# Optimization experiments

Hardware: AMD Instinct MI355X
Metric: run time of the kernel (lower is better)

## Reference

```python
import jax, jax.numpy as jnp
import numpy as np

N = 100000      # nodes
E = 1600000     # edges
IN_C = 128
HID = 64
OUT_C = 40
LAYERS = 8
ALPHA = 0.1
THETA = 0.5
BN_EPS = 1e-5


def setup_inputs() -> dict:
    key = jax.random.key(0)
    ks = jax.random.split(key, 8)
    x = jax.random.normal(ks[0], (N, IN_C), jnp.float32)
    edge_index = jax.random.randint(ks[1], (2, E), 0, N, dtype=jnp.int64)
    W0 = jax.random.normal(ks[2], (IN_C, HID), jnp.float32) / np.sqrt(IN_C).astype(np.float32)
    b0 = jnp.zeros((HID,), jnp.float32)
    convW = jax.random.normal(ks[3], (LAYERS, HID, HID), jnp.float32) / np.sqrt(HID).astype(np.float32)
    bn_gamma = jnp.ones((LAYERS, HID), jnp.float32)
    bn_beta = jnp.zeros((LAYERS, HID), jnp.float32)
    W_out = jax.random.normal(ks[4], (HID, OUT_C), jnp.float32) / np.sqrt(HID).astype(np.float32)
    b_out = jnp.zeros((OUT_C,), jnp.float32)
    return dict(x=x, edge_index=edge_index, W0=W0, b0=b0, convW=convW,
                bn_gamma=bn_gamma, bn_beta=bn_beta, W_out=W_out, b_out=b_out)


def _gcn_norm(edge_index, n):
    # gcn_norm with improved=False, add_self_loops=True (pyg default)
    loop = jnp.arange(n, dtype=edge_index.dtype)
    row = jnp.concatenate([edge_index[0], loop])
    col = jnp.concatenate([edge_index[1], loop])
    deg = jnp.zeros((n,), jnp.float32).at[col].add(1.0)  # deg >= 1 (self loops)
    dinv = jax.lax.rsqrt(deg)
    w = dinv[row] * dinv[col]
    return row, col, w


def reference(x, edge_index, W0, b0, convW, bn_gamma, bn_beta, W_out, b_out):
    n = x.shape[0]
    row, col, w = _gcn_norm(edge_index, n)
    # dropout in eval mode -> identity
    h = jax.nn.relu(x @ W0 + b0)
    h0 = h
    for i in range(LAYERS):
        beta = float(np.log(THETA / (i + 1) + 1.0))  # GCN2Conv beta for layer i+1
        # adj_t @ h: adj_t = transpose of normalized adjacency -> out[col] += w * h[row]
        agg = jnp.zeros_like(h).at[col].add(w[:, None] * h[row])
        s = (1.0 - ALPHA) * agg + ALPHA * h0              # initial residual
        s = (1.0 - beta) * s + beta * (s @ convW[i])      # identity mapping (shared_weights)
        mu = s.mean(axis=0)
        var = s.var(axis=0)                               # batchnorm (batch stats, biased var)
        s = (s - mu) * jax.lax.rsqrt(var + BN_EPS) * bn_gamma[i] + bn_beta[i]
        h = jax.nn.relu(s)
    return h @ W_out + b_out
```

## Files before the change

kernel.cpp:

```cpp
#include <hip/hip_runtime.h>
#include <math.h>

#define NTHREADS 256
#define IN_C 128
#define HID 64
#define OUT_C 40
#define N_LAYERS 8
#define ALPHA 0.1f
#define BN_EPS 1e-5f
#define BKT_SHIFT 9

typedef float f32x4 __attribute__((ext_vector_type(4)));
typedef _Float16 f16;
typedef _Float16 f16x4 __attribute__((ext_vector_type(4)));
typedef _Float16 f16x8 __attribute__((ext_vector_type(8)));

__device__ __forceinline__ f32x4 ld4(const float* p) { return *(const f32x4*)p; }

__device__ __forceinline__ f32x4 ldh4(const f16* p) {
  f16x4 v = *(const f16x4*)p;
  return __builtin_convertvector(v, f32x4);
}

__device__ __forceinline__ f32x4 bnrelu(f32x4 v, f32x4 k1, f32x4 k2) {
  f32x4 r = v * k1 + k2;
  r.x = fmaxf(r.x, 0.f); r.y = fmaxf(r.y, 0.f);
  r.z = fmaxf(r.z, 0.f); r.w = fmaxf(r.w, 0.f);
  return r;
}

__device__ __forceinline__ f32x4 xreduce(f32x4 v) {
  v.x += __shfl_xor(v.x, 16); v.y += __shfl_xor(v.y, 16);
  v.z += __shfl_xor(v.z, 16); v.w += __shfl_xor(v.w, 16);
  v.x += __shfl_xor(v.x, 32); v.y += __shfl_xor(v.y, 32);
  v.z += __shfl_xor(v.z, 32); v.w += __shfl_xor(v.w, 32);
  return v;
}


__global__ void k_zero(float* __restrict__ sumP, float* __restrict__ sumsqP,
                       f16* __restrict__ svpad, int* __restrict__ bcnt) {
  int i = blockIdx.x * NTHREADS + threadIdx.x;
  if (i < N_LAYERS * 1024) { sumP[i] = 0.f; sumsqP[i] = 0.f; }
  if (i < 256) {
    f16x4 z = {(f16)0.f, (f16)0.f, (f16)0.f, (f16)0.f};
    ((f16x4*)svpad)[i] = z;
  }
  if (blockIdx.x == 0 && threadIdx.x < 256) bcnt[threadIdx.x] = 0;
}

__global__ __launch_bounds__(NTHREADS) void k_bhist(
    const int* __restrict__ col, int* __restrict__ bcnt, int E, int nb) {
  __shared__ int lhist[512];
  int t = threadIdx.x;
  for (int i = t; i < nb; i += NTHREADS) lhist[i] = 0;
  __syncthreads();
  int start = blockIdx.x * 4096;
  int end = min(E, start + 4096);
  for (int e = start + t; e < end; e += NTHREADS)
    atomicAdd(&lhist[col[e] >> BKT_SHIFT], 1);
  __syncthreads();
  for (int i = t; i < nb; i += NTHREADS) {
    int c = lhist[i];
    if (c) atomicAdd(&bcnt[i], c);
  }
}

__global__ void k_bscan(const int* __restrict__ bcnt, int* __restrict__ bbase,
                        int* __restrict__ bcur, int* __restrict__ offs,
                        int nb, int n, int E) {
  __shared__ int sh[256];
  int t = threadIdx.x;
  int v = (t < nb) ? bcnt[t] : 0;
  sh[t] = v;
  __syncthreads();
  int run = v;
  for (int d = 1; d < 256; d <<= 1) {
    int add = (t >= d) ? sh[t - d] : 0;
    __syncthreads();
    run += add;
    sh[t] = run;
    __syncthreads();
  }
  if (t < nb) {
    bbase[t] = run - v;
    bcur[t] = run - v;
  }
  if (t == 0) {
    bbase[nb] = E;
    offs[n] = E;
  }
}

__global__ __launch_bounds__(NTHREADS) void k_bucketA(
    const int* __restrict__ row, const int* __restrict__ col,
    int* __restrict__ bcur, long long* __restrict__ tmp, int E, int nb) {
  __shared__ int lhist[512];
  __shared__ int lbase[512];
  int t = threadIdx.x;
  for (int i = t; i < nb; i += NTHREADS) lhist[i] = 0;
  __syncthreads();
  int start = blockIdx.x * 4096;
  int end = min(E, start + 4096);
  for (int e = start + t; e < end; e += NTHREADS)
    atomicAdd(&lhist[col[e] >> BKT_SHIFT], 1);
  __syncthreads();
  for (int i = t; i < nb; i += NTHREADS) {
    int c = lhist[i];
    lbase[i] = c ? atomicAdd(&bcur[i], c) : 0;
    lhist[i] = 0;
  }
  __syncthreads();
  for (int e = start + t; e < end; e += NTHREADS) {
    int cl = col[e];
    int b = cl >> BKT_SHIFT;
    int slot = atomicAdd(&lhist[b], 1);
    tmp[lbase[b] + slot] = ((long long)cl << 32) | (unsigned int)row[e];
  }
}

__global__ __launch_bounds__(512) void k_bucketB(
    const long long* __restrict__ tmp, const int* __restrict__ bbase,
    int* __restrict__ offs, float* __restrict__ dinv,
    int* __restrict__ ew, int n) {
  __shared__ int lcnt[512];
  __shared__ int lcur[512];
  int b = blockIdx.x;
  int t = threadIdx.x;
  int lo = b << BKT_SHIFT;
  int s = bbase[b], e2 = bbase[b + 1];
  lcnt[t] = 0;
  __syncthreads();
  for (int j = s + t; j < e2; j += 512)
    atomicAdd(&lcnt[(int)(tmp[j] >> 32) - lo], 1);
  __syncthreads();
  int v = lcnt[t];
  int run = v;
  for (int d = 1; d < 512; d <<= 1) {
    int add = (t >= d) ? lcnt[t - d] : 0;
    __syncthreads();
    run += add;
    lcnt[t] = run;
    __syncthreads();
  }
  int node = lo + t;
  int myoff = s + run - v;
  if (node < n) {
    offs[node] = myoff;
    dinv[node] = rsqrtf((float)v + 1.0f);
  }
  lcur[t] = myoff;
  __syncthreads();
  for (int j = s + t; j < e2; j += 512) {
    long long r = tmp[j];
    int cl = (int)(r >> 32);
    int pos = atomicAdd(&lcur[cl - lo], 1);
    ew[pos] = (int)(r & 0xffffffffLL);
  }
}

__global__ void k_gemm0(
    const float* __restrict__ x, const float* __restrict__ W0,
    const float* __restrict__ b0, const float* __restrict__ dinv,
    f16* __restrict__ h016, f16* __restrict__ hp, int n) {
  int t = threadIdx.x;
  int lane = t & 63, wid = t >> 6;
  int lm = lane & 15, lk = lane >> 4;
  f16x8 bf[4][4];
  float bv[4];
#pragma unroll
  for (int nt = 0; nt < 4; nt++) {
    int c = nt * 16 + lm;
    bv[nt] = b0[c];
#pragma unroll
    for (int ks = 0; ks < 4; ks++) {
#pragma unroll
      for (int i = 0; i < 8; i++) {
        bf[nt][ks][i] = (f16)W0[(ks * 32 + lk * 8 + i) * HID + c];
      }
    }
  }
  int nblk = (n + 15) >> 4;
  for (int blk = blockIdx.x * 4 + wid; blk < nblk; blk += gridDim.x * 4) {
    int r0 = blk * 16;
    int rA = min(r0 + lm, n - 1);
    const float* xr = x + (size_t)rA * IN_C + lk * 8;
    f16x8 af[4];
#pragma unroll
    for (int ks = 0; ks < 4; ks++) {
      f32x4 lo = ld4(xr + ks * 32);
      f32x4 hi = ld4(xr + ks * 32 + 4);
      f16x4 l16 = __builtin_convertvector(lo, f16x4);
      f16x4 h16 = __builtin_convertvector(hi, f16x4);
#pragma unroll
      for (int i = 0; i < 4; i++) { af[ks][i] = l16[i]; af[ks][4 + i] = h16[i]; }
    }
    float dv[4];
#pragma unroll
    for (int reg = 0; reg < 4; reg++)
      dv[reg] = dinv[min(r0 + lk * 4 + reg, n - 1)];
#pragma unroll
    for (int nt = 0; nt < 4; nt++) {
      f32x4 z = {0.f, 0.f, 0.f, 0.f};
      z = __builtin_amdgcn_mfma_f32_16x16x32_f16(af[0], bf[nt][0], z, 0, 0, 0);
      z = __builtin_amdgcn_mfma_f32_16x16x32_f16(af[1], bf[nt][1], z, 0, 0, 0);
      z = __builtin_amdgcn_mfma_f32_16x16x32_f16(af[2], bf[nt][2], z, 0, 0, 0);
      z = __builtin_amdgcn_mfma_f32_16x16x32_f16(af[3], bf[nt][3], z, 0, 0, 0);
#pragma unroll
      for (int reg = 0; reg < 4; reg++) {
        int r = r0 + lk * 4 + reg;
        if (r < n) {
          float v = fmaxf(z[reg] + bv[nt], 0.f);
          h016[(size_t)r * HID + nt * 16 + lm] = (f16)v;
          hp[(size_t)r * HID + nt * 16 + lm] = (f16)(dv[reg] * v);
        }
      }
    }
  }
}

__global__ void k_gather(
    const f16* __restrict__ hp, const f16* __restrict__ h0,
    const float* __restrict__ dinv, const int* __restrict__ offs,
    const int* __restrict__ ew, f16* __restrict__ sv, int n) {
  int t = threadIdx.x;
  int lane = t & 63;
  int eg = lane >> 4, li = lane & 15, c4 = li << 2;
  int i = blockIdx.x * 16 + (t >> 6) * 4 + eg;
  if (i >= n) return;
  int jb = offs[i], je = offs[i + 1];
  float di = dinv[i];
  f16x4 hs16 = *(const f16x4*)(hp + (size_t)i * HID + c4);
  f16x4 h016v = *(const f16x4*)(h0 + (size_t)i * HID + c4);
  f32x4 acc = {0.f, 0.f, 0.f, 0.f};
  int j = jb;
  for (; j + 8 <= je; j += 8) {
    int q0 = ew[j + 0];
    int q1 = ew[j + 1];
    int q2 = ew[j + 2];
    int q3 = ew[j + 3];
    int q4 = ew[j + 4];
    int q5 = ew[j + 5];
    int q6 = ew[j + 6];
    int q7 = ew[j + 7];
    f16x4 u0 = *(const f16x4*)(hp + (size_t)q0 * HID + c4);
    f16x4 u1 = *(const f16x4*)(hp + (size_t)q1 * HID + c4);
    f16x4 u2 = *(const f16x4*)(hp + (size_t)q2 * HID + c4);
    f16x4 u3 = *(const f16x4*)(hp + (size_t)q3 * HID + c4);
    f16x4 u4 = *(const f16x4*)(hp + (size_t)q4 * HID + c4);
    f16x4 u5 = *(const f16x4*)(hp + (size_t)q5 * HID + c4);
    f16x4 u6 = *(const f16x4*)(hp + (size_t)q6 * HID + c4);
    f16x4 u7 = *(const f16x4*)(hp + (size_t)q7 * HID + c4);
    acc += __builtin_convertvector(u0, f32x4);
    acc += __builtin_convertvector(u1, f32x4);
    acc += __builtin_convertvector(u2, f32x4);
    acc += __builtin_convertvector(u3, f32x4);
    acc += __builtin_convertvector(u4, f32x4);
    acc += __builtin_convertvector(u5, f32x4);
    acc += __builtin_convertvector(u6, f32x4);
    acc += __builtin_convertvector(u7, f32x4);
  }
  for (; j < je; j++) {
    acc += ldh4(hp + (size_t)ew[j] * HID + c4);
  }
  f32x4 hs = __builtin_convertvector(hs16, f32x4);
  f32x4 h0v = __builtin_convertvector(h016v, f32x4);
  f32x4 sval = (1.f - ALPHA) * (di * (acc + hs)) + ALPHA * h0v;
  *(f16x4*)(sv + (size_t)i * HID + c4) = __builtin_convertvector(sval, f16x4);
}

__global__ __launch_bounds__(NTHREADS) void k_conv(
    const f16* __restrict__ sv, const float* __restrict__ Wl,
    f16* __restrict__ sout, float* __restrict__ sumL,
    float* __restrict__ sumsqL, float beta, int n) {
  __shared__ __align__(16) float Wsh[HID * HID];
  __shared__ f32x4 red4[2][4][16];
  int t = threadIdx.x;
  for (int m = t; m < HID * HID / 4; m += NTHREADS) {
    f32x4 wv = ((const f32x4*)Wl)[m];
    wv *= beta;
    int base = m * 4;
    int k = base >> 6, c0 = base & 63;
    if (k >= c0 && k < c0 + 4) wv[k - c0] += (1.f - beta);
    ((f32x4*)Wsh)[m] = wv;
  }
  __syncthreads();
  int lane = t & 63, wid = t >> 6;
  int lm = lane & 15, lk = lane >> 4;
  f16x8 bf[4][2];
#pragma unroll
  for (int nt = 0; nt < 4; nt++) {
#pragma unroll
    for (int ks = 0; ks < 2; ks++) {
      int c = nt * 16 + lm;
#pragma unroll
      for (int i = 0; i < 8; i++) {
        int k = ks * 32 + lk * 8 + i;
        bf[nt][ks][i] = (f16)Wsh[k * HID + c];
      }
    }
  }
  float ssum[4] = {0.f, 0.f, 0.f, 0.f}, ssq[4] = {0.f, 0.f, 0.f, 0.f};
  int nblk = (n + 15) >> 4;
  for (int blk = blockIdx.x * 4 + wid; blk < nblk; blk += gridDim.x * 4) {
    int r0 = blk * 16;
    const f16* ap = sv + (size_t)(r0 + lm) * HID + lk * 8;
    f16x8 a0 = *(const f16x8*)(ap);
    f16x8 a1 = *(const f16x8*)(ap + 32);
#pragma unroll
    for (int nt = 0; nt < 4; nt++) {
      f32x4 z = {0.f, 0.f, 0.f, 0.f};
      z = __builtin_amdgcn_mfma_f32_16x16x32_f16(a0, bf[nt][0], z, 0, 0, 0);
      z = __builtin_amdgcn_mfma_f32_16x16x32_f16(a1, bf[nt][1], z, 0, 0, 0);
#pragma unroll
      for (int reg = 0; reg < 4; reg++) {
        int r = r0 + lk * 4 + reg;
        if (r < n) {
          float v = z[reg];
          sout[(size_t)r * HID + nt * 16 + lm] = (f16)v;
          ssum[nt] += v;
          ssq[nt] += v * v;
        }
      }
    }
  }
  f32x4 sumv = {ssum[0], ssum[1], ssum[2], ssum[3]};
  f32x4 sqv = {ssq[0], ssq[1], ssq[2], ssq[3]};
  sumv = xreduce(sumv);
  sqv = xreduce(sqv);
  if (lk == 0) { red4[0][wid][lm] = sumv; red4[1][wid][lm] = sqv; }
  __syncthreads();
  if (t < 16) {
    f32x4 a = red4[0][0][t] + red4[0][1][t] + red4[0][2][t] + red4[0][3][t];
    f32x4 b = red4[1][0][t] + red4[1][1][t] + red4[1][2][t] + red4[1][3][t];
    int js = (blockIdx.x & 15) * 64;
    atomicAdd(&sumL[js + 0 * 16 + t], a.x);
    atomicAdd(&sumL[js + 1 * 16 + t], a.y);
    atomicAdd(&sumL[js + 2 * 16 + t], a.z);
    atomicAdd(&sumL[js + 3 * 16 + t], a.w);
    atomicAdd(&sumsqL[js + 0 * 16 + t], b.x);
    atomicAdd(&sumsqL[js + 1 * 16 + t], b.y);
    atomicAdd(&sumsqL[js + 2 * 16 + t], b.z);
    atomicAdd(&sumsqL[js + 3 * 16 + t], b.w);
  }
}

__device__ __forceinline__ void stats_to_lds(
    const float* __restrict__ sumL, const float* __restrict__ sumsqL,
    const float* __restrict__ gamma_l, const float* __restrict__ beta_l,
    float* ms, int t, int n) {
  if (t < 64) {
    float s = 0.f, sq = 0.f;
#pragma unroll
    for (int j = 0; j < 16; j++) {
      s += sumL[j * 64 + t];
      sq += sumsqL[j * 64 + t];
    }
    float mu = s / (float)n;
    float var = sq / (float)n - mu * mu;
    float iv = rsqrtf(var + BN_EPS);
    float k1 = iv * gamma_l[t];
    ms[t] = k1;
    ms[64 + t] = beta_l[t] - mu * k1;
  }
  __syncthreads();
}

__global__ __launch_bounds__(NTHREADS) void k_bnrelu(
    const f16* __restrict__ s, const float* __restrict__ sumL,
    const float* __restrict__ sumsqL, const float* __restrict__ gamma_l,
    const float* __restrict__ beta_l, const float* __restrict__ dinv,
    f16* __restrict__ hp, int n) {
  __shared__ __align__(16) float ms[128];
  int t = threadIdx.x;
  stats_to_lds(sumL, sumsqL, gamma_l, beta_l, ms, t, n);
  int idx = blockIdx.x * NTHREADS + t;
  if (idx < n * (HID / 4)) {
    int c4 = idx & 15;
    int row = idx >> 4;
    f32x4 v = ldh4(s + (size_t)idx * 4);
    f32x4 k1 = *(const f32x4*)(ms + c4 * 4);
    f32x4 k2 = *(const f32x4*)(ms + 64 + c4 * 4);
    v = bnrelu(v, k1, k2);
    float di = dinv[row];
    v = di * v;
    ((f16x4*)hp)[idx] = __builtin_convertvector(v, f16x4);
  }
}

__global__ __launch_bounds__(NTHREADS) void k_out(
    const f16* __restrict__ s, const float* __restrict__ sumL,
    const float* __restrict__ sumsqL, const float* __restrict__ gamma_l,
    const float* __restrict__ beta_l, const float* __restrict__ Wout,
    const float* __restrict__ bout, float* __restrict__ out, int n) {
  __shared__ float Ws[HID * OUT_C];
  __shared__ float bs[OUT_C];
  __shared__ __align__(16) float ms[128];
  int t = threadIdx.x;
  for (int m = t; m < HID * OUT_C; m += NTHREADS) Ws[m] = Wout[m];
  if (t < OUT_C) bs[t] = bout[t];
  stats_to_lds(sumL, sumsqL, gamma_l, beta_l, ms, t, n);
  int idx = blockIdx.x * NTHREADS + t;
  if (idx < n * OUT_C) {
    int row = idx / OUT_C;
    int c = idx - row * OUT_C;
    float acc = bs[c];
    const f16* sr = s + (size_t)row * HID;
    for (int kk = 0; kk < HID / 4; kk++) {
      f32x4 a = ldh4(sr + kk * 4);
      f32x4 k1 = *(const f32x4*)(ms + kk * 4);
      f32x4 k2 = *(const f32x4*)(ms + 64 + kk * 4);
      a = bnrelu(a, k1, k2);
      int k = kk * 4;
      acc += a.x * Ws[(k + 0) * OUT_C + c] + a.y * Ws[(k + 1) * OUT_C + c] +
             a.z * Ws[(k + 2) * OUT_C + c] + a.w * Ws[(k + 3) * OUT_C + c];
    }
    out[idx] = acc;
  }
}


extern "C" void kernel_launch(void* const* d_in, const int* in_sizes, int n_in,
                              void* d_out, int out_size, void* d_ws, size_t ws_size,
                              hipStream_t stream) {
  const float* x = (const float*)d_in[0];
  const int* ei = (const int*)d_in[1];
  const float* W0 = (const float*)d_in[2];
  const float* b0 = (const float*)d_in[3];
  const float* convW = (const float*)d_in[4];
  const float* bn_gamma = (const float*)d_in[5];
  const float* bn_beta = (const float*)d_in[6];
  const float* W_out = (const float*)d_in[7];
  const float* b_out = (const float*)d_in[8];
  float* out = (float*)d_out;

  int n = in_sizes[0] / IN_C;
  int E = in_sizes[1] / 2;
  const int* row = ei;
  const int* col = ei + E;
  int NB = (n + (1 << BKT_SHIFT) - 1) >> BKT_SHIFT;

  char* w = (char*)d_ws;
  auto alloc = [&](size_t bytes) {
    char* p = w;
    w += (bytes + 255) & ~(size_t)255;
    return p;
  };
  float* dinv    = (float*)alloc((size_t)n * 4);
  int*   offs    = (int*)alloc((size_t)(n + 1) * 4);
  int*   bcnt    = (int*)alloc(512 * 4);
  int*   bbase   = (int*)alloc(512 * 4);
  int*   bcur    = (int*)alloc(512 * 4);
  int*   ew      = (int*)alloc((size_t)E * 4);
  long long* tmp = (long long*)alloc((size_t)E * 8);
  f16*   h016    = (f16*)alloc((size_t)n * HID * 2);
  f16*   hp      = (f16*)alloc((size_t)n * HID * 2);
  f16*   sv      = (f16*)alloc((size_t)(n + 16) * HID * 2);
  f16*   sb      = (f16*)alloc((size_t)n * HID * 2);
  float* sumP    = (float*)alloc((size_t)N_LAYERS * 1024 * 4);
  float* sumsqP  = (float*)alloc((size_t)N_LAYERS * 1024 * 4);

  int gE4 = (E + 4095) / 4096;
  int gRow = (n + 15) / 16;
  int gConv = (gRow + 3) / 4;
  int gV = (n * (HID / 4) + NTHREADS - 1) / NTHREADS;

  k_zero<<<33, NTHREADS, 0, stream>>>(sumP, sumsqP, sv + (size_t)n * HID, bcnt);
  k_bhist<<<gE4, NTHREADS, 0, stream>>>(col, bcnt, E, NB);
  k_bscan<<<1, 256, 0, stream>>>(bcnt, bbase, bcur, offs, NB, n, E);
  k_bucketA<<<gE4, NTHREADS, 0, stream>>>(row, col, bcur, tmp, E, NB);
  k_bucketB<<<NB, 512, 0, stream>>>(tmp, bbase, offs, dinv, ew, n);

  k_gemm0<<<512, NTHREADS, 0, stream>>>(x, W0, b0, dinv, h016, hp, n);

  for (int l = 0; l < N_LAYERS; l++) {
    float beta = logf(0.5f / (float)(l + 1) + 1.0f);
    if (l > 0) {
      k_bnrelu<<<gV, NTHREADS, 0, stream>>>(
          sb, sumP + (size_t)(l - 1) * 1024, sumsqP + (size_t)(l - 1) * 1024,
          bn_gamma + (l - 1) * HID, bn_beta + (l - 1) * HID, dinv, hp, n);
    }
    k_gather<<<gRow, NTHREADS, 0, stream>>>(hp, h016, dinv, offs, ew, sv, n);
    k_conv<<<gConv, NTHREADS, 0, stream>>>(sv, convW + (size_t)l * HID * HID,
                                           sb, sumP + (size_t)l * 1024,
                                           sumsqP + (size_t)l * 1024, beta, n);
  }

  k_out<<<((size_t)n * OUT_C + NTHREADS - 1) / NTHREADS, NTHREADS, 0, stream>>>(
      sb, sumP + (size_t)7 * 1024, sumsqP + (size_t)7 * 1024,
      bn_gamma + 7 * HID, bn_beta + 7 * HID, W_out, b_out, out, n);
}
```

Baseline: 693.1 us.

## Compute output projection with MFMA f16 instead of scalar per-element loop

Rewrites the final output kernel so each wavefront handles 16-row blocks and computes the 64x40 projection with mfma_f32_16x16x32_f16, keeping W_out fragments in registers. The old version used one thread per output element, re-reading the row of s and W_out from LDS 64 times per output. The new version also launches a grid-stride kernel with the conv grid size. In exchange, W_out and the post-BN activations are rounded to f16 before the multiply, which costs some precision, and it pads 40 columns up to 48.

```diff
diff --git a/kernel.cpp b/kernel.cpp
--- a/kernel.cpp
+++ b/kernel.cpp
@@ -393,29 +393,61 @@
     const float* __restrict__ sumsqL, const float* __restrict__ gamma_l,
     const float* __restrict__ beta_l, const float* __restrict__ Wout,
     const float* __restrict__ bout, float* __restrict__ out, int n) {
-  __shared__ float Ws[HID * OUT_C];
-  __shared__ float bs[OUT_C];
   __shared__ __align__(16) float ms[128];
   int t = threadIdx.x;
-  for (int m = t; m < HID * OUT_C; m += NTHREADS) Ws[m] = Wout[m];
-  if (t < OUT_C) bs[t] = bout[t];
   stats_to_lds(sumL, sumsqL, gamma_l, beta_l, ms, t, n);
-  int idx = blockIdx.x * NTHREADS + t;
-  if (idx < n * OUT_C) {
-    int row = idx / OUT_C;
-    int c = idx - row * OUT_C;
-    float acc = bs[c];
-    const f16* sr = s + (size_t)row * HID;
-    for (int kk = 0; kk < HID / 4; kk++) {
-      f32x4 a = ldh4(sr + kk * 4);
-      f32x4 k1 = *(const f32x4*)(ms + kk * 4);
-      f32x4 k2 = *(const f32x4*)(ms + 64 + kk * 4);
-      a = bnrelu(a, k1, k2);
-      int k = kk * 4;
-      acc += a.x * Ws[(k + 0) * OUT_C + c] + a.y * Ws[(k + 1) * OUT_C + c] +
-             a.z * Ws[(k + 2) * OUT_C + c] + a.w * Ws[(k + 3) * OUT_C + c];
-    }
-    out[idx] = acc;
+  int lane = t & 63, wid = t >> 6;
+  int lm = lane & 15, lk = lane >> 4;
+  f16x8 bf[3][2];
+  float bv[3];
+#pragma unroll
+  for (int nt = 0; nt < 3; nt++) {
+    int c = nt * 16 + lm;
+    bv[nt] = (c < OUT_C) ? bout[c] : 0.f;
+#pragma unroll
+    for (int ks = 0; ks < 2; ks++) {
+#pragma unroll
+      for (int i = 0; i < 8; i++) {
+        int k = ks * 32 + lk * 8 + i;
+        bf[nt][ks][i] = (c < OUT_C) ? (f16)Wout[k * OUT_C + c] : (f16)0.f;
+      }
+    }
+  }
+  float k1a[8], k2a[8], k1b[8], k2b[8];
+#pragma unroll
+  for (int i = 0; i < 8; i++) {
+    k1a[i] = ms[lk * 8 + i];
+    k2a[i] = ms[64 + lk * 8 + i];
+    k1b[i] = ms[32 + lk * 8 + i];
+    k2b[i] = ms[64 + 32 + lk * 8 + i];
+  }
+  int nblk = (n + 15) >> 4;
+  for (int blk = blockIdx.x * 4 + wid; blk < nblk; blk += gridDim.x * 4) {
+    int r0 = blk * 16;
+    int rA = min(r0 + lm, n - 1);
+    const f16* sr = s + (size_t)rA * HID + lk * 8;
+    f16x8 s0 = *(const f16x8*)(sr);
+    f16x8 s1 = *(const f16x8*)(sr + 32);
+    f16x8 a0, a1;
+#pragma unroll
+    for (int i = 0; i < 8; i++) {
+      a0[i] = (f16)fmaxf((float)s0[i] * k1a[i] + k2a[i], 0.f);
+      a1[i] = (f16)fmaxf((float)s1[i] * k1b[i] + k2b[i], 0.f);
+    }
+#pragma unroll
+    for (int nt = 0; nt < 3; nt++) {
+      int c = nt * 16 + lm;
+      f32x4 z = {0.f, 0.f, 0.f, 0.f};
+      z = __builtin_amdgcn_mfma_f32_16x16x32_f16(a0, bf[nt][0], z, 0, 0, 0);
+      z = __builtin_amdgcn_mfma_f32_16x16x32_f16(a1, bf[nt][1], z, 0, 0, 0);
+#pragma unroll
+      for (int reg = 0; reg < 4; reg++) {
+        int r = r0 + lk * 4 + reg;
+        if (r < n && c < OUT_C) {
+          out[(size_t)r * OUT_C + c] = z[reg] + bv[nt];
+        }
+      }
+    }
   }
 }
 
@@ -486,7 +518,7 @@
                                            sumsqP + (size_t)l * 1024, beta, n);
   }
 
-  k_out<<<((size_t)n * OUT_C + NTHREADS - 1) / NTHREADS, NTHREADS, 0, stream>>>(
+  k_out<<<gConv, NTHREADS, 0, stream>>>(
       sb, sumP + (size_t)7 * 1024, sumsqP + (size_t)7 * 1024,
       bn_gamma + 7 * HID, bn_beta + 7 * HID, W_out, b_out, out, n);
 }
```

Measured after the change: 655.4 us. 5.4% less time.
